# Optimization experiments

Measured on AMD Instinct MI355X. Metric: run time of the kernel, lower is better.

The kernel has to match this reference:

```python
import jax, jax.numpy as jnp
import numpy as np

NUM_HEADS = 16
HEAD_DIM = 256
FFN_HIDDEN = 512
NUM_USER_HEADS = 8
EPS = 1e-6
BATCH = 8192


def _make_mask(num_heads, head_dim, num_user_heads):
    m = np.ones((num_heads, head_dim), dtype=np.float32)
    sub = head_dim // num_heads
    m[:num_user_heads, num_user_heads * sub:] = 0.0
    return jnp.asarray(m)


def setup_inputs() -> dict:
    key = jax.random.key(0)
    ks = jax.random.split(key, 6)
    x = jax.random.normal(ks[0], (BATCH, NUM_HEADS, HEAD_DIM), dtype=jnp.float32)
    norm1_w = jnp.ones((HEAD_DIM,), dtype=jnp.float32)
    norm2_w = jnp.ones((HEAD_DIM,), dtype=jnp.float32)
    s_in = 1.0 / np.sqrt(HEAD_DIM)
    s_hid = 1.0 / np.sqrt(FFN_HIDDEN)
    w1 = jax.random.normal(ks[1], (NUM_HEADS, HEAD_DIM, FFN_HIDDEN), dtype=jnp.float32) * s_in
    w3 = jax.random.normal(ks[2], (NUM_HEADS, HEAD_DIM, FFN_HIDDEN), dtype=jnp.float32) * s_in
    w2 = jax.random.normal(ks[3], (NUM_HEADS, FFN_HIDDEN, HEAD_DIM), dtype=jnp.float32) * s_hid
    mask = _make_mask(NUM_HEADS, HEAD_DIM, NUM_USER_HEADS)
    return {"x": x, "norm1_w": norm1_w, "norm2_w": norm2_w,
            "w1": w1, "w3": w3, "w2": w2, "mask": mask}


def _rmsnorm(x, w):
    # x: (B,N,D), w: (D,)
    rms = jax.lax.rsqrt(jnp.mean(x * x, axis=-1, keepdims=True) + EPS)
    return x * rms * w


def _head_mixing(x):
    # Parameter-free cross-head sub-dim exchange:
    # mixed[:, i, j*sub:(j+1)*sub] = x[:, j, i*sub:(i+1)*sub]
    B, N, D = x.shape
    sub = D // N
    return x.reshape(B, N, N, sub).transpose(0, 2, 1, 3).reshape(B, N, D)


def reference(x, norm1_w, norm2_w, w1, w3, w2, mask):
    # UI-decoupled HeadMixing: mask zeroes item-head info flowing into user heads
    mixed = _head_mixing(_rmsnorm(x, norm1_w)) * mask[None, :, :]
    p = mixed + x
    # per-head SwiGLU FFN
    h = _rmsnorm(p, norm2_w)
    a = jnp.einsum('bnd,ndh->bnh', h, w1)  # gate
    b = jnp.einsum('bnd,ndh->bnh', h, w3)  # value
    ffn = jnp.einsum('bnh,nhd->bnd', jax.nn.silu(a) * b, w2)
    return ffn + p
```

## Files before the change

kernel.cpp:

```cpp
#include <hip/hip_runtime.h>
#include <hip/hip_bf16.h>
#include <cstdint>

#define B_SZ 8192
#define NH 16
#define HD 256
#define FH 512

typedef __bf16 bf16x8 __attribute__((ext_vector_type(8)));
typedef float f32x4 __attribute__((ext_vector_type(4)));

__device__ __forceinline__ void lds_load16(const void* g, void* l) {
  __builtin_amdgcn_global_load_lds(
      (const __attribute__((address_space(1))) unsigned char*)g,
      (__attribute__((address_space(3))) unsigned char*)l, 16, 0, 0);
}

__global__ __launch_bounds__(256) void wcvt_kernel(const float* __restrict__ w1,
                                                   const float* __restrict__ w3,
                                                   const float* __restrict__ w2,
                                                   __bf16* __restrict__ w1t,
                                                   __bf16* __restrict__ w3t,
                                                   __bf16* __restrict__ w2t) {
  int bid = blockIdx.x;
  const float* src;
  __bf16* dst;
  int K, N;
  if (bid < 2048)      { src = w1; dst = w1t; K = 256; N = 512; }
  else if (bid < 4096) { src = w3; dst = w3t; K = 256; N = 512; bid -= 2048; }
  else                 { src = w2; dst = w2t; K = 512; N = 256; bid -= 4096; }
  const int tiles_n = N >> 5, tiles_k = K >> 5;
  const int per_head = tiles_n * tiles_k;
  const int head = bid / per_head;
  const int rem = bid - head * per_head;
  const int tk = rem / tiles_n;
  const int tn = rem - tk * tiles_n;
  __shared__ float tile[32][33];
  const float* s = src + ((size_t)head * K + tk * 32) * N + tn * 32;
  const int r = threadIdx.x >> 3;
  const int c4 = (threadIdx.x & 7) * 4;
  float4 v = *(const float4*)(s + (size_t)r * N + c4);
  tile[r][c4 + 0] = v.x; tile[r][c4 + 1] = v.y;
  tile[r][c4 + 2] = v.z; tile[r][c4 + 3] = v.w;
  __syncthreads();
  __bf16 o[4] __attribute__((aligned(8)));
  #pragma unroll
  for (int j = 0; j < 4; ++j) o[j] = (__bf16)tile[c4 + j][r];
  __bf16* d = dst + ((size_t)head * N + tn * 32 + r) * K + tk * 32 + c4;
  *(uint2*)d = *(uint2*)o;
}

__global__ __launch_bounds__(256) void prep_kernel(const float* __restrict__ x,
                                                   const float* __restrict__ n1w,
                                                   const float* __restrict__ n2w,
                                                   const float* __restrict__ mask,
                                                   __bf16* __restrict__ p_ws,
                                                   __bf16* __restrict__ h_ws) {
  const int b = blockIdx.x;
  const int t = threadIdx.x;
  const int g = t >> 4;
  const int li = t & 15;
  __shared__ float xs[16 * 260];
  __shared__ float rms1s[16];
  const float* xb = x + (size_t)b * (NH * HD);

  float xv[16];
  float ss = 0.f;
  #pragma unroll
  for (int j = 0; j < 4; ++j) {
    float4 v = *(const float4*)(xb + g * HD + li * 16 + j * 4);
    *(float4*)(xs + g * 260 + li * 16 + j * 4) = v;
    xv[j * 4 + 0] = v.x; xv[j * 4 + 1] = v.y;
    xv[j * 4 + 2] = v.z; xv[j * 4 + 3] = v.w;
    ss += v.x * v.x + v.y * v.y + v.z * v.z + v.w * v.w;
  }
  #pragma unroll
  for (int d = 1; d < 16; d <<= 1) ss += __shfl_xor(ss, d);
  if (li == 0) rms1s[g] = rsqrtf(ss * (1.f / 256.f) + 1e-6f);
  __syncthreads();

  const float r1 = rms1s[li];
  float pv[16];
  float ss2 = 0.f;
  #pragma unroll
  for (int j = 0; j < 4; ++j) {
    float4 sv = *(const float4*)(xs + li * 260 + g * 16 + j * 4);
    float s4[4] = {sv.x, sv.y, sv.z, sv.w};
    #pragma unroll
    for (int q = 0; q < 4; ++q) {
      const int k = j * 4 + q;
      const int c = li * 16 + k;
      const float mixed = s4[q] * r1 * n1w[g * 16 + k] * mask[g * HD + c];
      const float p = mixed + xv[k];
      pv[k] = p;
      ss2 += p * p;
    }
  }
  #pragma unroll
  for (int d = 1; d < 16; d <<= 1) ss2 += __shfl_xor(ss2, d);
  const float r2 = rsqrtf(ss2 * (1.f / 256.f) + 1e-6f);

  __bf16 pb[16] __attribute__((aligned(16)));
  __bf16 hv[16] __attribute__((aligned(16)));
  #pragma unroll
  for (int k = 0; k < 16; ++k) {
    const int c = li * 16 + k;
    pb[k] = (__bf16)pv[k];
    hv[k] = (__bf16)(pv[k] * r2 * n2w[c]);
  }
  __bf16* pp = p_ws + ((size_t)g * B_SZ + b) * HD + li * 16;
  *(uint4*)(pp + 0) = *(uint4*)(pb + 0);
  *(uint4*)(pp + 8) = *(uint4*)(pb + 8);
  __bf16* hp = h_ws + ((size_t)g * B_SZ + b) * HD + li * 16;
  *(uint4*)(hp + 0) = *(uint4*)(hv + 0);
  *(uint4*)(hp + 8) = *(uint4*)(hv + 8);
}

__global__ __launch_bounds__(256) void gemm1_kernel(const __bf16* __restrict__ h_ws,
                                                    const __bf16* __restrict__ w1t,
                                                    const __bf16* __restrict__ w3t,
                                                    __bf16* __restrict__ s_ws) {
  const int bid = blockIdx.x;
  const int nt = bid >> 10;
  const int q = bid & 1023;
  const int head = q >> 6, mt = q & 63;
  const int row0 = mt * 128, col0 = nt * 64;
  const int t = threadIdx.x;
  const int wv = t >> 6, lane = t & 63;
  const int wm = wv >> 1, wn = wv & 1;
  const int mlane = lane & 15, quad = lane >> 4;

  __shared__ __bf16 As[2 * 128 * 32];
  __shared__ __bf16 B1s[2 * 64 * 32];
  __shared__ __bf16 B3s[2 * 64 * 32];

  const __bf16* Ab = h_ws + ((size_t)head * B_SZ + row0) * HD;
  const __bf16* B1b = w1t + ((size_t)head * FH + col0) * HD;
  const __bf16* B3b = w3t + ((size_t)head * FH + col0) * HD;

  f32x4 accg[4][2], accv[4][2];
  #pragma unroll
  for (int i = 0; i < 4; ++i)
    #pragma unroll
    for (int j = 0; j < 2; ++j) {
      accg[i][j] = (f32x4){0.f, 0.f, 0.f, 0.f};
      accv[i][j] = (f32x4){0.f, 0.f, 0.f, 0.f};
    }

  const int arow = t >> 2;
  const int acol = (t & 3) * 8;

  for (int kk = 0; kk < 4; ++kk) {
    const int k0 = kk * 64;
    lds_load16(Ab + (size_t)arow * HD + k0 + acol,             As + wv * 512);
    lds_load16(Ab + (size_t)(arow + 64) * HD + k0 + acol,      As + 2048 + wv * 512);
    lds_load16(Ab + (size_t)arow * HD + k0 + 32 + acol,        As + 4096 + wv * 512);
    lds_load16(Ab + (size_t)(arow + 64) * HD + k0 + 32 + acol, As + 4096 + 2048 + wv * 512);
    lds_load16(B1b + (size_t)arow * HD + k0 + acol,            B1s + wv * 512);
    lds_load16(B1b + (size_t)arow * HD + k0 + 32 + acol,       B1s + 2048 + wv * 512);
    lds_load16(B3b + (size_t)arow * HD + k0 + acol,            B3s + wv * 512);
    lds_load16(B3b + (size_t)arow * HD + k0 + 32 + acol,       B3s + 2048 + wv * 512);
    __syncthreads();

    #pragma unroll
    for (int ks = 0; ks < 2; ++ks) {
      bf16x8 a[4], b1[2], b3[2];
      #pragma unroll
      for (int i = 0; i < 4; ++i)
        a[i] = *(const bf16x8*)(As + ks * 4096 + (wm * 64 + i * 16 + mlane) * 32 + quad * 8);
      #pragma unroll
      for (int j = 0; j < 2; ++j) {
        b1[j] = *(const bf16x8*)(B1s + ks * 2048 + (wn * 32 + j * 16 + mlane) * 32 + quad * 8);
        b3[j] = *(const bf16x8*)(B3s + ks * 2048 + (wn * 32 + j * 16 + mlane) * 32 + quad * 8);
      }
      #pragma unroll
      for (int i = 0; i < 4; ++i)
        #pragma unroll
        for (int j = 0; j < 2; ++j) {
          accg[i][j] = __builtin_amdgcn_mfma_f32_16x16x32_bf16(a[i], b1[j], accg[i][j], 0, 0, 0);
          accv[i][j] = __builtin_amdgcn_mfma_f32_16x16x32_bf16(a[i], b3[j], accv[i][j], 0, 0, 0);
        }
    }
    __syncthreads();
  }

  __bf16* Sb = s_ws + ((size_t)head * B_SZ + row0) * FH + col0;
  #pragma unroll
  for (int i = 0; i < 4; ++i)
    #pragma unroll
    for (int j = 0; j < 2; ++j)
      #pragma unroll
      for (int r = 0; r < 4; ++r) {
        const int rr = wm * 64 + i * 16 + quad * 4 + r;
        const int cc = wn * 32 + j * 16 + mlane;
        const float gg = accg[i][j][r];
        const float vvv = accv[i][j][r];
        const float s = gg / (1.f + __expf(-gg)) * vvv;
        Sb[(size_t)rr * FH + cc] = (__bf16)s;
      }
}

__global__ __launch_bounds__(256) void gemm2_kernel(const __bf16* __restrict__ s_ws,
                                                    const __bf16* __restrict__ w2t,
                                                    const __bf16* __restrict__ p_ws,
                                                    float* __restrict__ out) {
  const int bid = blockIdx.x;
  const int nt = bid >> 10;
  const int q = bid & 1023;
  const int head = q >> 6, mt = q & 63;
  const int row0 = mt * 128, col0 = nt * 128;
  const int t = threadIdx.x;
  const int wv = t >> 6, lane = t & 63;
  const int wm = wv >> 1, wn = wv & 1;
  const int mlane = lane & 15, quad = lane >> 4;

  __shared__ __bf16 As[2 * 128 * 32];
  __shared__ __bf16 Bs[2 * 128 * 32];

  const __bf16* Ab = s_ws + ((size_t)head * B_SZ + row0) * FH;
  const __bf16* Bb = w2t + ((size_t)head * HD + col0) * FH;

  f32x4 acc[4][4];
  #pragma unroll
  for (int i = 0; i < 4; ++i)
    #pragma unroll
    for (int j = 0; j < 4; ++j) acc[i][j] = (f32x4){0.f, 0.f, 0.f, 0.f};

  const int arow = t >> 2;
  const int acol = (t & 3) * 8;

  for (int kk = 0; kk < 8; ++kk) {
    const int k0 = kk * 64;
    lds_load16(Ab + (size_t)arow * FH + k0 + acol,             As + wv * 512);
    lds_load16(Ab + (size_t)(arow + 64) * FH + k0 + acol,      As + 2048 + wv * 512);
    lds_load16(Ab + (size_t)arow * FH + k0 + 32 + acol,        As + 4096 + wv * 512);
    lds_load16(Ab + (size_t)(arow + 64) * FH + k0 + 32 + acol, As + 4096 + 2048 + wv * 512);
    lds_load16(Bb + (size_t)arow * FH + k0 + acol,             Bs + wv * 512);
    lds_load16(Bb + (size_t)(arow + 64) * FH + k0 + acol,      Bs + 2048 + wv * 512);
    lds_load16(Bb + (size_t)arow * FH + k0 + 32 + acol,        Bs + 4096 + wv * 512);
    lds_load16(Bb + (size_t)(arow + 64) * FH + k0 + 32 + acol, Bs + 4096 + 2048 + wv * 512);
    __syncthreads();

    #pragma unroll
    for (int ks = 0; ks < 2; ++ks) {
      bf16x8 a[4], b[4];
      #pragma unroll
      for (int i = 0; i < 4; ++i)
        a[i] = *(const bf16x8*)(As + ks * 4096 + (wm * 64 + i * 16 + mlane) * 32 + quad * 8);
      #pragma unroll
      for (int j = 0; j < 4; ++j)
        b[j] = *(const bf16x8*)(Bs + ks * 4096 + (wn * 64 + j * 16 + mlane) * 32 + quad * 8);
      #pragma unroll
      for (int i = 0; i < 4; ++i)
        #pragma unroll
        for (int j = 0; j < 4; ++j)
          acc[i][j] = __builtin_amdgcn_mfma_f32_16x16x32_bf16(a[i], b[j], acc[i][j], 0, 0, 0);
    }
    __syncthreads();
  }

  const __bf16* Pb = p_ws + ((size_t)head * B_SZ + row0) * HD + col0;
  float* Ob = out + (size_t)row0 * (NH * HD) + head * HD + col0;
  #pragma unroll
  for (int i = 0; i < 4; ++i)
    #pragma unroll
    for (int j = 0; j < 4; ++j)
      #pragma unroll
      for (int r = 0; r < 4; ++r) {
        const int rr = wm * 64 + i * 16 + quad * 4 + r;
        const int cc = wn * 64 + j * 16 + mlane;
        Ob[(size_t)rr * (NH * HD) + cc] =
            acc[i][j][r] + (float)Pb[(size_t)rr * HD + cc];
      }
}

extern "C" void kernel_launch(void* const* d_in, const int* in_sizes, int n_in,
                              void* d_out, int out_size, void* d_ws, size_t ws_size,
                              hipStream_t stream) {
  const float* x    = (const float*)d_in[0];
  const float* n1w  = (const float*)d_in[1];
  const float* n2w  = (const float*)d_in[2];
  const float* w1   = (const float*)d_in[3];
  const float* w3   = (const float*)d_in[4];
  const float* w2   = (const float*)d_in[5];
  const float* mask = (const float*)d_in[6];
  float* out = (float*)d_out;

  char* ws = (char*)d_ws;
  __bf16* p_ws = (__bf16*)(ws + 0);
  __bf16* h_ws = (__bf16*)(ws + 67108864);
  __bf16* s_ws = (__bf16*)(ws + 134217728);
  __bf16* w1t  = (__bf16*)(ws + 268435456);
  __bf16* w3t  = (__bf16*)(ws + 272629760);
  __bf16* w2t  = (__bf16*)(ws + 276824064);

  wcvt_kernel<<<6144, 256, 0, stream>>>(w1, w3, w2, w1t, w3t, w2t);
  prep_kernel<<<8192, 256, 0, stream>>>(x, n1w, n2w, mask, p_ws, h_ws);
  gemm1_kernel<<<8192, 256, 0, stream>>>(h_ws, w1t, w3t, s_ws);
  gemm2_kernel<<<2048, 256, 0, stream>>>(s_ws, w2t, p_ws, out);
}
```

Baseline: 486.4 us.

## Fuse gate/value GEMM, SwiGLU and down-projection into one per-stripe FFN kernel

```diff
diff --git a/kernel.cpp b/kernel.cpp
--- a/kernel.cpp
+++ b/kernel.cpp
@@ -6,6 +6,7 @@
 #define NH 16
 #define HD 256
 #define FH 512
+#define BR 64
 
 typedef __bf16 bf16x8 __attribute__((ext_vector_type(8)));
 typedef float f32x4 __attribute__((ext_vector_type(4)));
@@ -116,162 +117,123 @@
   *(uint4*)(hp + 8) = *(uint4*)(hv + 8);
 }
 
-__global__ __launch_bounds__(256) void gemm1_kernel(const __bf16* __restrict__ h_ws,
-                                                    const __bf16* __restrict__ w1t,
-                                                    const __bf16* __restrict__ w3t,
-                                                    __bf16* __restrict__ s_ws) {
+__global__ __launch_bounds__(256) void ffn_kernel(const __bf16* __restrict__ h_ws,
+                                                  const __bf16* __restrict__ w1t,
+                                                  const __bf16* __restrict__ w3t,
+                                                  const __bf16* __restrict__ w2t,
+                                                  const __bf16* __restrict__ p_ws,
+                                                  float* __restrict__ out) {
   const int bid = blockIdx.x;
-  const int nt = bid >> 10;
-  const int q = bid & 1023;
-  const int head = q >> 6, mt = q & 63;
-  const int row0 = mt * 128, col0 = nt * 64;
+  const int head = (bid & 7) | (((bid >> 3) & 1) << 3);
+  const int stripe = bid >> 4;
+  const int r0 = stripe * BR;
   const int t = threadIdx.x;
   const int wv = t >> 6, lane = t & 63;
-  const int wm = wv >> 1, wn = wv & 1;
   const int mlane = lane & 15, quad = lane >> 4;
 
-  __shared__ __bf16 As[2 * 128 * 32];
-  __shared__ __bf16 B1s[2 * 64 * 32];
-  __shared__ __bf16 B3s[2 * 64 * 32];
-
-  const __bf16* Ab = h_ws + ((size_t)head * B_SZ + row0) * HD;
-  const __bf16* B1b = w1t + ((size_t)head * FH + col0) * HD;
-  const __bf16* B3b = w3t + ((size_t)head * FH + col0) * HD;
-
-  f32x4 accg[4][2], accv[4][2];
-  #pragma unroll
-  for (int i = 0; i < 4; ++i)
-    #pragma unroll
-    for (int j = 0; j < 2; ++j) {
-      accg[i][j] = (f32x4){0.f, 0.f, 0.f, 0.f};
-      accv[i][j] = (f32x4){0.f, 0.f, 0.f, 0.f};
-    }
-
-  const int arow = t >> 2;
-  const int acol = (t & 3) * 8;
-
-  for (int kk = 0; kk < 4; ++kk) {
-    const int k0 = kk * 64;
-    lds_load16(Ab + (size_t)arow * HD + k0 + acol,             As + wv * 512);
-    lds_load16(Ab + (size_t)(arow + 64) * HD + k0 + acol,      As + 2048 + wv * 512);
-    lds_load16(Ab + (size_t)arow * HD + k0 + 32 + acol,        As + 4096 + wv * 512);
-    lds_load16(Ab + (size_t)(arow + 64) * HD + k0 + 32 + acol, As + 4096 + 2048 + wv * 512);
-    lds_load16(B1b + (size_t)arow * HD + k0 + acol,            B1s + wv * 512);
-    lds_load16(B1b + (size_t)arow * HD + k0 + 32 + acol,       B1s + 2048 + wv * 512);
-    lds_load16(B3b + (size_t)arow * HD + k0 + acol,            B3s + wv * 512);
-    lds_load16(B3b + (size_t)arow * HD + k0 + 32 + acol,       B3s + 2048 + wv * 512);
+  __shared__ __bf16 Hs[BR * HD];
+  __shared__ __bf16 Sc[BR * 64];
+
+  const __bf16* Hb = h_ws + ((size_t)head * B_SZ + r0) * HD;
+  {
+    const int rloc = lane >> 5;
+    const int ch = lane & 31;
+    #pragma unroll
+    for (int i = 0; i < 8; ++i) {
+      const int row = wv * 16 + i * 2 + rloc;
+      const int gch = ch ^ (row & 15);
+      lds_load16(Hb + (size_t)row * HD + gch * 8,
+                 Hs + (wv * 16 + i * 2) * HD);
+    }
+  }
+  __syncthreads();
+
+  f32x4 oacc[4][4];
+  #pragma unroll
+  for (int mt = 0; mt < 4; ++mt)
+    #pragma unroll
+    for (int nt = 0; nt < 4; ++nt) oacc[mt][nt] = (f32x4){0.f, 0.f, 0.f, 0.f};
+
+  const __bf16* A2base = w2t + ((size_t)head * HD + wv * 64) * FH;
+
+  for (int hc = 0; hc < 8; ++hc) {
+    const __bf16* A1 = w1t + ((size_t)head * FH + hc * 64 + wv * 16 + mlane) * HD;
+    const __bf16* A3 = w3t + ((size_t)head * FH + hc * 64 + wv * 16 + mlane) * HD;
+    f32x4 g[4], v[4];
+    #pragma unroll
+    for (int nt = 0; nt < 4; ++nt) {
+      g[nt] = (f32x4){0.f, 0.f, 0.f, 0.f};
+      v[nt] = (f32x4){0.f, 0.f, 0.f, 0.f};
+    }
+    #pragma unroll
+    for (int ks = 0; ks < 8; ++ks) {
+      bf16x8 a1 = *(const bf16x8*)(A1 + ks * 32 + quad * 8);
+      bf16x8 a3 = *(const bf16x8*)(A3 + ks * 32 + quad * 8);
+      #pragma unroll
+      for (int nt = 0; nt < 4; ++nt) {
+        const int row = nt * 16 + mlane;
+        const int ch = (ks * 4 + quad) ^ (row & 15);
+        bf16x8 b = *(const bf16x8*)(Hs + row * HD + ch * 8);
+        g[nt] = __builtin_amdgcn_mfma_f32_16x16x32_bf16(a1, b, g[nt], 0, 0, 0);
+        v[nt] = __builtin_amdgcn_mfma_f32_16x16x32_bf16(a3, b, v[nt], 0, 0, 0);
+      }
+    }
+
     __syncthreads();
-
-    #pragma unroll
-    for (int ks = 0; ks < 2; ++ks) {
-      bf16x8 a[4], b1[2], b3[2];
-      #pragma unroll
-      for (int i = 0; i < 4; ++i)
-        a[i] = *(const bf16x8*)(As + ks * 4096 + (wm * 64 + i * 16 + mlane) * 32 + quad * 8);
-      #pragma unroll
-      for (int j = 0; j < 2; ++j) {
-        b1[j] = *(const bf16x8*)(B1s + ks * 2048 + (wn * 32 + j * 16 + mlane) * 32 + quad * 8);
-        b3[j] = *(const bf16x8*)(B3s + ks * 2048 + (wn * 32 + j * 16 + mlane) * 32 + quad * 8);
+    #pragma unroll
+    for (int nt = 0; nt < 4; ++nt) {
+      const int row = nt * 16 + mlane;
+      __bf16 sv[4] __attribute__((aligned(8)));
+      #pragma unroll
+      for (int r = 0; r < 4; ++r) {
+        const float gg = g[nt][r];
+        sv[r] = (__bf16)(gg / (1.f + __expf(-gg)) * v[nt][r]);
       }
-      #pragma unroll
-      for (int i = 0; i < 4; ++i)
-        #pragma unroll
-        for (int j = 0; j < 2; ++j) {
-          accg[i][j] = __builtin_amdgcn_mfma_f32_16x16x32_bf16(a[i], b1[j], accg[i][j], 0, 0, 0);
-          accv[i][j] = __builtin_amdgcn_mfma_f32_16x16x32_bf16(a[i], b3[j], accv[i][j], 0, 0, 0);
-        }
-    }
-    __syncthreads();
-  }
-
-  __bf16* Sb = s_ws + ((size_t)head * B_SZ + row0) * FH + col0;
-  #pragma unroll
-  for (int i = 0; i < 4; ++i)
-    #pragma unroll
-    for (int j = 0; j < 2; ++j)
-      #pragma unroll
-      for (int r = 0; r < 4; ++r) {
-        const int rr = wm * 64 + i * 16 + quad * 4 + r;
-        const int cc = wn * 32 + j * 16 + mlane;
-        const float gg = accg[i][j][r];
-        const float vvv = accv[i][j][r];
-        const float s = gg / (1.f + __expf(-gg)) * vvv;
-        Sb[(size_t)rr * FH + cc] = (__bf16)s;
-      }
-}
-
-__global__ __launch_bounds__(256) void gemm2_kernel(const __bf16* __restrict__ s_ws,
-                                                    const __bf16* __restrict__ w2t,
-                                                    const __bf16* __restrict__ p_ws,
-                                                    float* __restrict__ out) {
-  const int bid = blockIdx.x;
-  const int nt = bid >> 10;
-  const int q = bid & 1023;
-  const int head = q >> 6, mt = q & 63;
-  const int row0 = mt * 128, col0 = nt * 128;
-  const int t = threadIdx.x;
-  const int wv = t >> 6, lane = t & 63;
-  const int wm = wv >> 1, wn = wv & 1;
-  const int mlane = lane & 15, quad = lane >> 4;
-
-  __shared__ __bf16 As[2 * 128 * 32];
-  __shared__ __bf16 Bs[2 * 128 * 32];
-
-  const __bf16* Ab = s_ws + ((size_t)head * B_SZ + row0) * FH;
-  const __bf16* Bb = w2t + ((size_t)head * HD + col0) * FH;
-
-  f32x4 acc[4][4];
-  #pragma unroll
-  for (int i = 0; i < 4; ++i)
-    #pragma unroll
-    for (int j = 0; j < 4; ++j) acc[i][j] = (f32x4){0.f, 0.f, 0.f, 0.f};
-
-  const int arow = t >> 2;
-  const int acol = (t & 3) * 8;
-
-  for (int kk = 0; kk < 8; ++kk) {
-    const int k0 = kk * 64;
-    lds_load16(Ab + (size_t)arow * FH + k0 + acol,             As + wv * 512);
-    lds_load16(Ab + (size_t)(arow + 64) * FH + k0 + acol,      As + 2048 + wv * 512);
-    lds_load16(Ab + (size_t)arow * FH + k0 + 32 + acol,        As + 4096 + wv * 512);
-    lds_load16(Ab + (size_t)(arow + 64) * FH + k0 + 32 + acol, As + 4096 + 2048 + wv * 512);
-    lds_load16(Bb + (size_t)arow * FH + k0 + acol,             Bs + wv * 512);
-    lds_load16(Bb + (size_t)(arow + 64) * FH + k0 + acol,      Bs + 2048 + wv * 512);
-    lds_load16(Bb + (size_t)arow * FH + k0 + 32 + acol,        Bs + 4096 + wv * 512);
-    lds_load16(Bb + (size_t)(arow + 64) * FH + k0 + 32 + acol, Bs + 4096 + 2048 + wv * 512);
+      const int boff = wv * 32 + quad * 8;
+      const int ph = ((boff >> 4) ^ (row & 7));
+      char* dst = (char*)Sc + row * 128 + ph * 16 + (boff & 15);
+      *(uint2*)dst = *(uint2*)sv;
+    }
     __syncthreads();
 
     #pragma unroll
     for (int ks = 0; ks < 2; ++ks) {
       bf16x8 a[4], b[4];
       #pragma unroll
-      for (int i = 0; i < 4; ++i)
-        a[i] = *(const bf16x8*)(As + ks * 4096 + (wm * 64 + i * 16 + mlane) * 32 + quad * 8);
-      #pragma unroll
-      for (int j = 0; j < 4; ++j)
-        b[j] = *(const bf16x8*)(Bs + ks * 4096 + (wn * 64 + j * 16 + mlane) * 32 + quad * 8);
-      #pragma unroll
-      for (int i = 0; i < 4; ++i)
+      for (int mt = 0; mt < 4; ++mt)
+        a[mt] = *(const bf16x8*)(A2base + (size_t)(mt * 16 + mlane) * FH +
+                                 hc * 64 + ks * 32 + quad * 8);
+      #pragma unroll
+      for (int nt = 0; nt < 4; ++nt) {
+        const int row = nt * 16 + mlane;
+        const int ch = (ks * 4 + quad) ^ (row & 7);
+        b[nt] = *(const bf16x8*)(Sc + row * 64 + ch * 8);
+      }
+      #pragma unroll
+      for (int mt = 0; mt < 4; ++mt)
         #pragma unroll
-        for (int j = 0; j < 4; ++j)
-          acc[i][j] = __builtin_amdgcn_mfma_f32_16x16x32_bf16(a[i], b[j], acc[i][j], 0, 0, 0);
-    }
-    __syncthreads();
-  }
-
-  const __bf16* Pb = p_ws + ((size_t)head * B_SZ + row0) * HD + col0;
-  float* Ob = out + (size_t)row0 * (NH * HD) + head * HD + col0;
-  #pragma unroll
-  for (int i = 0; i < 4; ++i)
-    #pragma unroll
-    for (int j = 0; j < 4; ++j)
-      #pragma unroll
-      for (int r = 0; r < 4; ++r) {
-        const int rr = wm * 64 + i * 16 + quad * 4 + r;
-        const int cc = wn * 64 + j * 16 + mlane;
-        Ob[(size_t)rr * (NH * HD) + cc] =
-            acc[i][j][r] + (float)Pb[(size_t)rr * HD + cc];
-      }
+        for (int nt = 0; nt < 4; ++nt)
+          oacc[mt][nt] = __builtin_amdgcn_mfma_f32_16x16x32_bf16(a[mt], b[nt], oacc[mt][nt], 0, 0, 0);
+    }
+  }
+
+  const __bf16* Pb = p_ws + ((size_t)head * B_SZ + r0) * HD;
+  float* Ob = out + (size_t)r0 * (NH * HD) + head * HD;
+  #pragma unroll
+  for (int mt = 0; mt < 4; ++mt)
+    #pragma unroll
+    for (int nt = 0; nt < 4; ++nt) {
+      const int row = nt * 16 + mlane;
+      const int oc = wv * 64 + mt * 16 + quad * 4;
+      __bf16 pv[4] __attribute__((aligned(8)));
+      *(uint2*)pv = *(const uint2*)(Pb + (size_t)row * HD + oc);
+      float4 o;
+      o.x = oacc[mt][nt][0] + (float)pv[0];
+      o.y = oacc[mt][nt][1] + (float)pv[1];
+      o.z = oacc[mt][nt][2] + (float)pv[2];
+      o.w = oacc[mt][nt][3] + (float)pv[3];
+      *(float4*)(Ob + (size_t)row * (NH * HD) + oc) = o;
+    }
 }
 
 extern "C" void kernel_launch(void* const* d_in, const int* in_sizes, int n_in,
@@ -289,13 +251,11 @@
   char* ws = (char*)d_ws;
   __bf16* p_ws = (__bf16*)(ws + 0);
   __bf16* h_ws = (__bf16*)(ws + 67108864);
-  __bf16* s_ws = (__bf16*)(ws + 134217728);
-  __bf16* w1t  = (__bf16*)(ws + 268435456);
-  __bf16* w3t  = (__bf16*)(ws + 272629760);
-  __bf16* w2t  = (__bf16*)(ws + 276824064);
+  __bf16* w1t  = (__bf16*)(ws + 134217728);
+  __bf16* w3t  = (__bf16*)(ws + 138412032);
+  __bf16* w2t  = (__bf16*)(ws + 142606336);
 
   wcvt_kernel<<<6144, 256, 0, stream>>>(w1, w3, w2, w1t, w3t, w2t);
   prep_kernel<<<8192, 256, 0, stream>>>(x, n1w, n2w, mask, p_ws, h_ws);
-  gemm1_kernel<<<8192, 256, 0, stream>>>(h_ws, w1t, w3t, s_ws);
-  gemm2_kernel<<<2048, 256, 0, stream>>>(s_ws, w2t, p_ws, out);
-}
+  ffn_kernel<<<2048, 256, 0, stream>>>(h_ws, w1t, w3t, w2t, p_ws, out);
+}
```

New measurement: 524.4 us. 1.08x slower.
